# Kernel optimization log

Measured on AMD Instinct MI355X. Metric: run time of the kernel, lower is better.

The kernel has to match this reference:

```python
import jax, jax.numpy as jnp
import numpy as np

EPS = 1e-5
C = 64  # in_channels == feat_channels == out_channels


def _ln(x, g, b):
    m = jnp.mean(x, axis=-1, keepdims=True)
    v = jnp.mean(jnp.square(x - m), axis=-1, keepdims=True)
    return (x - m) * jax.lax.rsqrt(v + EPS) * g + b


def setup_inputs() -> dict:
    key = jax.random.key(0)
    ks = jax.random.split(key, 10)
    bs, nc, H, W = 8, 80, 256, 256
    d = {
        "feat": jax.random.normal(ks[0], (bs, C, H, W), jnp.float32),
        "head": jax.random.normal(ks[1], (bs, nc, C, 1), jnp.float32),
        "pred": jax.random.normal(ks[2], (bs, nc, H // 2, W // 2), jnp.float32),
        # linear transforms (stored [in, out], applied as x @ W + b)
        "W_pred_t": jax.random.normal(ks[3], (C, 2 * C), jnp.float32) * 0.05,
        "b_pred_t": jnp.zeros((2 * C,), jnp.float32),
        "W_head_t": jax.random.normal(ks[4], (C, 2 * C), jnp.float32) * 0.05,
        "b_head_t": jnp.zeros((2 * C,), jnp.float32),
        "W_pred_g": jax.random.normal(ks[5], (C, C), jnp.float32) * 0.05,
        "b_pred_g": jnp.zeros((C,), jnp.float32),
        "W_head_g": jax.random.normal(ks[6], (C, C), jnp.float32) * 0.05,
        "b_head_g": jnp.zeros((C,), jnp.float32),
        "W_fc": jax.random.normal(ks[7], (C, C), jnp.float32) * 0.05,
        "b_fc": jnp.zeros((C,), jnp.float32),
        # layernorm params
        "g_pin": jnp.ones((C,), jnp.float32), "be_pin": jnp.zeros((C,), jnp.float32),
        "g_hin": jnp.ones((C,), jnp.float32), "be_hin": jnp.zeros((C,), jnp.float32),
        "g_pout": jnp.ones((C,), jnp.float32), "be_pout": jnp.zeros((C,), jnp.float32),
        "g_hout": jnp.ones((C,), jnp.float32), "be_hout": jnp.zeros((C,), jnp.float32),
        "g_fc": jnp.ones((C,), jnp.float32), "be_fc": jnp.zeros((C,), jnp.float32),
    }
    return d


def reference(feat, head, pred,
              W_pred_t, b_pred_t, W_head_t, b_head_t,
              W_pred_g, b_pred_g, W_head_g, b_head_g,
              W_fc, b_fc,
              g_pin, be_pin, g_hin, be_hin,
              g_pout, be_pout, g_hout, be_hout,
              g_fc, be_fc):
    bs, nc = head.shape[:2]
    H, W = feat.shape[2], feat.shape[3]
    pred_up = jax.image.resize(pred, (bs, nc, H, W), method="bilinear")
    pred_up = jax.nn.sigmoid(pred_up)
    # head-aware feature assembly: [bs, nc, C]
    assemble = jnp.einsum("bnhw,bchw->bnc", pred_up, feat)
    a = assemble.reshape(-1, C)                      # [BN, C]
    BN = a.shape[0]
    # head: [bs, nc, C, kk] -> [BN, kk, C]
    hd = jnp.transpose(head.reshape(bs, nc, C, -1), (0, 1, 3, 2)).reshape(BN, -1, C)

    pf = a @ W_pred_t + b_pred_t                     # [BN, 2C]
    pf_in, pf_out = pf[:, :C], pf[:, C:]
    hf = hd @ W_head_t + b_head_t                    # [BN, kk, 2C]
    hf_in, hf_out = hf[..., :C], hf[..., C:]

    gate = hf_in * pf_in[:, None, :]                 # [BN, kk, C]
    head_gate = jax.nn.sigmoid(_ln(gate @ W_head_g + b_head_g, g_hin, be_hin))
    pred_gate = jax.nn.sigmoid(_ln(gate @ W_pred_g + b_pred_g, g_pin, be_pin))

    hf_out = _ln(hf_out, g_hout, be_hout)
    pf_out = _ln(pf_out, g_pout, be_pout)

    upd = pred_gate * pf_out[:, None, :] + head_gate * hf_out
    upd = jax.nn.relu(_ln(upd @ W_fc + b_fc, g_fc, be_fc))
    upd = upd.reshape(bs, nc, -1, C)
    upd = jnp.transpose(upd, (0, 1, 3, 2)).reshape(bs, nc, C, 1, 1)
    return upd
```

## Files before the change

### kernel.cpp

```cpp
#include <hip/hip_runtime.h>
#include <hip/hip_bf16.h>
#include <hip/hip_fp16.h>


using bf16x8 = __attribute__((ext_vector_type(8))) short;
using f32x4  = __attribute__((ext_vector_type(4))) float;

#define SCHED_FENCE() __builtin_amdgcn_sched_barrier(0)
#define LGKM_BARRIER() do { \
  asm volatile("s_waitcnt lgkmcnt(0)" ::: "memory"); \
  __builtin_amdgcn_s_barrier(); } while (0)

__device__ __forceinline__ unsigned pk2(float lo, float hi) {
  union { __hip_bfloat162 h2; unsigned u; } cv;
  cv.h2 = __float22bfloat162_rn(make_float2(lo, hi));
  return cv.u;
}
__device__ __forceinline__ float sigAB(float a, float b) {
  return __builtin_amdgcn_rcpf(1.0f + __builtin_amdgcn_exp2f(-0.36067376f * a - 1.08202128f * b));
}
__device__ __forceinline__ float sigBA(float a, float b) {
  return __builtin_amdgcn_rcpf(1.0f + __builtin_amdgcn_exp2f(-1.08202128f * a - 0.36067376f * b));
}

__global__ __launch_bounds__(256, 4) void k_assemble_half(
    const float* __restrict__ feat, const float* __restrict__ pred,
    __half* __restrict__ partial) {
  __shared__ __align__(16) unsigned short Pfrag[20 * 64 * 8];

  const int bid = blockIdx.x;
  const int wg  = (bid & 7) * 512 + (bid >> 3);
  const int half = wg & 1;
  const int h    = (wg >> 1) & 255;
  const int b    = wg >> 9;

  const int tid = threadIdx.x;
  const int gg = tid & 15, nbp = tid >> 4;
  const int wid = tid >> 6, l = tid & 63;
  const int ch16 = l & 15, kg = l >> 4, c0 = wid << 4;

  const int j = h >> 1;
  int r0, r1; float wy0, wy1;
  if ((h & 1) == 0) { r0 = (j > 0) ? j - 1 : 0; r1 = j; wy0 = 0.25f; wy1 = 0.75f; }
  else              { r0 = j; r1 = (j < 127) ? j + 1 : 127; wy0 = 0.75f; wy1 = 0.25f; }

  const int cbase = half << 6;
  const int csc   = 64 - half;
  const float* pbat = pred + (((size_t)(b * 80)) << 14);

  float4 p0[5], p1[5];
  #pragma unroll
  for (int i = 0; i < 5; ++i) {
    const float* pb = pbat + (((size_t)(nbp + 16 * i)) << 14);
    p0[i] = *(const float4*)(pb + (r0 << 7) + cbase + 4 * gg);
    p1[i] = *(const float4*)(pb + (r1 << 7) + cbase + 4 * gg);
  }

  #pragma unroll
  for (int i = 0; i < 5; ++i) {
    const int n = nbp + 16 * i;
    const float* pb = pbat + (((size_t)n) << 14);
    const float sc = wy0 * pb[(r0 << 7) + csc] + wy1 * pb[(r1 << 7) + csc];
    const float y0 = wy0 * p0[i].x + wy1 * p1[i].x;
    const float y1 = wy0 * p0[i].y + wy1 * p1[i].y;
    const float y2 = wy0 * p0[i].z + wy1 * p1[i].z;
    const float y3 = wy0 * p0[i].w + wy1 * p1[i].w;
    float yl = __shfl_up(y3, 1, 16);
    float yr = __shfl_down(y0, 1, 16);
    if (gg == 0)  yl = half ? sc : y0;
    if (gg == 15) yr = half ? y3 : sc;
    float P[8];
    P[0] = sigAB(yl, y0); P[1] = sigBA(y0, y1);
    P[2] = sigAB(y0, y1); P[3] = sigBA(y1, y2);
    P[4] = sigAB(y1, y2); P[5] = sigBA(y2, y3);
    P[6] = sigAB(y2, y3); P[7] = sigBA(y3, yr);
    uint4 s;
    s.x = pk2(P[0], P[1]); s.y = pk2(P[2], P[3]);
    s.z = pk2(P[4], P[5]); s.w = pk2(P[6], P[7]);
    const int ks = gg >> 2, kgw = gg & 3;
    const int slot = kgw * 16 + ((nbp ^ ks ^ (kgw << 1)) & 15);
    *(uint4*)&Pfrag[(((ks * 5 + i) * 64) + slot) * 8] = s;
  }
  __syncthreads();

  const float* fb = feat + (((size_t)(b * 64 + c0 + ch16)) << 16) + h * 256 + (half << 7);
  f32x4 acc[5] = {};
  #pragma unroll
  for (int ks = 0; ks < 4; ++ks) {
    const int pw = ks * 32 + kg * 8;
    const float4 f0 = *(const float4*)(fb + pw);
    const float4 f1 = *(const float4*)(fb + pw + 4);
    union { uint4 u; bf16x8 v; } bu;
    bu.u.x = pk2(f0.x, f0.y); bu.u.y = pk2(f0.z, f0.w);
    bu.u.z = pk2(f1.x, f1.y); bu.u.w = pk2(f1.z, f1.w);
    const int slot = kg * 16 + ((ch16 ^ ks ^ (kg << 1)) & 15);
    #pragma unroll
    for (int m = 0; m < 5; ++m) {
      const bf16x8 af = *(const bf16x8*)&Pfrag[(((ks * 5 + m) * 64) + slot) * 8];
      acc[m] = __builtin_amdgcn_mfma_f32_16x16x32_bf16(af, bu.v, acc[m], 0, 0, 0);
    }
  }

  __half* po = partial + ((size_t)(b * 512 + h * 2 + half)) * (80 * 64);
  #pragma unroll
  for (int m = 0; m < 5; ++m) {
    #pragma unroll
    for (int q = 0; q < 4; ++q) {
      const int n = m * 16 + kg * 4 + q;
      po[n * 64 + c0 + ch16] = __float2half(acc[m][q]);
    }
  }
}

__global__ __launch_bounds__(256) void k_assemble_full(
    const float* __restrict__ feat, const float* __restrict__ pred,
    __half* __restrict__ partial) {
  __shared__ __align__(16) unsigned short Pfrag[40 * 64 * 8];

  const int tid = threadIdx.x;
  const int b  = blockIdx.x >> 7;
  const int rb = blockIdx.x & 127;
  const int wid = tid >> 6, l = tid & 63;
  const int ch16 = l & 15, kg = l >> 4;
  const int c0 = wid << 4;
  const int h0 = rb * 2;
  const int gg = tid & 31, nb = tid >> 5;

  f32x4 acc[5] = {};
  const float* fwave = feat + (((size_t)(b * 64 + c0 + ch16)) << 16);
  const float* pbat  = pred + (((size_t)(b * 80)) << 14);

  #pragma unroll
  for (int r = 0; r < 2; ++r) {
    const int h = h0 + r;
    const int j = h >> 1;
    int r0, r1; float wy0, wy1;
    if ((h & 1) == 0) { r0 = (j > 0) ? j - 1 : 0; r1 = j; wy0 = 0.25f; wy1 = 0.75f; }
    else              { r0 = j; r1 = (j < 127) ? j + 1 : 127; wy0 = 0.75f; wy1 = 0.25f; }

    float4 p0[10], p1[10];
    #pragma unroll
    for (int i = 0; i < 10; ++i) {
      const float* pb = pbat + (((size_t)(nb + 8 * i)) << 14);
      p0[i] = *(const float4*)(pb + (r0 << 7) + gg * 4);
      p1[i] = *(const float4*)(pb + (r1 << 7) + gg * 4);
    }
    SCHED_FENCE();

    const float* fb = fwave + h * 256;
    float4 f[16];
    #pragma unroll
    for (int ks = 0; ks < 8; ++ks) {
      const int pw = ks * 32 + kg * 8;
      f[2 * ks]     = *(const float4*)(fb + pw);
      f[2 * ks + 1] = *(const float4*)(fb + pw + 4);
    }
    SCHED_FENCE();

    #pragma unroll
    for (int i = 0; i < 10; ++i) {
      const int n = nb + 8 * i;
      const float y0 = wy0 * p0[i].x + wy1 * p1[i].x;
      const float y1 = wy0 * p0[i].y + wy1 * p1[i].y;
      const float y2 = wy0 * p0[i].z + wy1 * p1[i].z;
      const float y3 = wy0 * p0[i].w + wy1 * p1[i].w;
      float yl = __shfl_up(y3, 1, 64);   if (gg == 0)  yl = y0;
      float yr = __shfl_down(y0, 1, 64); if (gg == 31) yr = y3;
      float P[8];
      P[0] = sigAB(yl, y0); P[1] = sigBA(y0, y1);
      P[2] = sigAB(y0, y1); P[3] = sigBA(y1, y2);
      P[4] = sigAB(y1, y2); P[5] = sigBA(y2, y3);
      P[6] = sigAB(y2, y3); P[7] = sigBA(y3, yr);
      uint4 s;
      s.x = pk2(P[0], P[1]); s.y = pk2(P[2], P[3]);
      s.z = pk2(P[4], P[5]); s.w = pk2(P[6], P[7]);
      const int ks = gg >> 2, kgw = gg & 3;
      const int slot = kgw * 16 + (((n & 15) ^ ks ^ (kgw << 1)) & 15);
      *(uint4*)&Pfrag[(((ks * 5 + (n >> 4)) * 64) + slot) * 8] = s;
    }
    LGKM_BARRIER();

    #pragma unroll
    for (int ks = 0; ks < 8; ++ks) {
      const float4 f0 = f[2 * ks], f1 = f[2 * ks + 1];
      union { uint4 u; bf16x8 v; } bu;
      bu.u.x = pk2(f0.x, f0.y); bu.u.y = pk2(f0.z, f0.w);
      bu.u.z = pk2(f1.x, f1.y); bu.u.w = pk2(f1.z, f1.w);
      const int slot = kg * 16 + ((ch16 ^ ks ^ (kg << 1)) & 15);
      #pragma unroll
      for (int m = 0; m < 5; ++m) {
        const bf16x8 af = *(const bf16x8*)&Pfrag[(((ks * 5 + m) * 64) + slot) * 8];
        acc[m] = __builtin_amdgcn_mfma_f32_16x16x32_bf16(af, bu.v, acc[m], 0, 0, 0);
      }
    }
    LGKM_BARRIER();
  }

  __half* po = partial + ((size_t)(b * 128 + rb)) * (80 * 64);
  #pragma unroll
  for (int m = 0; m < 5; ++m) {
    #pragma unroll
    for (int q = 0; q < 4; ++q) {
      const int n = m * 16 + kg * 4 + q;
      po[n * 64 + c0 + ch16] = __float2half(acc[m][q]);
    }
  }
}

__device__ __forceinline__ float wred64(float v) {
  #pragma unroll
  for (int off = 32; off > 0; off >>= 1) v += __shfl_xor(v, off, 64);
  return v;
}
__device__ __forceinline__ float lnorm(float x, const float* __restrict__ g,
                                       const float* __restrict__ be, int l) {
  const float m = wred64(x) * 0.015625f;
  const float d = x - m;
  const float var = wred64(d * d) * 0.015625f;
  return d * rsqrtf(var + 1e-5f) * g[l] + be[l];
}
__device__ __forceinline__ float sigmf(float x) {
  return __builtin_amdgcn_rcpf(1.0f + __builtin_amdgcn_exp2f(-1.44269504f * x));
}

__global__ __launch_bounds__(256) void k_head(
    const __half* __restrict__ partial, const float* __restrict__ head,
    const float* __restrict__ Wpt, const float* __restrict__ bpt,
    const float* __restrict__ Wht, const float* __restrict__ bht,
    const float* __restrict__ Wpg, const float* __restrict__ bpg,
    const float* __restrict__ Whg, const float* __restrict__ bhg,
    const float* __restrict__ Wfc, const float* __restrict__ bfc,
    const float* __restrict__ g_pin, const float* __restrict__ be_pin,
    const float* __restrict__ g_hin, const float* __restrict__ be_hin,
    const float* __restrict__ g_pout, const float* __restrict__ be_pout,
    const float* __restrict__ g_hout, const float* __restrict__ be_hout,
    const float* __restrict__ g_fc, const float* __restrict__ be_fc,
    float* __restrict__ out, int npart) {
  __shared__ float red[4][64];
  __shared__ float buf[4][64];
  const int tid = threadIdx.x, c = tid & 63, q = tid >> 6;
  const int r = blockIdx.x;
  const int b = r / 80, n = r % 80;
  const int npq = npart >> 2;

  const __half* pp = partial + ((size_t)b * npart + (size_t)q * npq) * 5120 + n * 64 + c;
  float s = 0.f;
  #pragma unroll 8
  for (int jj = 0; jj < npq; ++jj) s += __half2float(pp[(size_t)jj * 5120]);
  red[q][c] = s;
  __syncthreads();

  if (q == 0) {
    const float a_c = red[0][c] + red[1][c] + red[2][c] + red[3][c];
    buf[0][c] = a_c;
    buf[1][c] = head[(size_t)r * 64 + c];

    float pf_in = bpt[c], pf_out = bpt[64 + c];
    float hf_in = bht[c], hf_out = bht[64 + c];
    #pragma unroll 8
    for (int k = 0; k < 64; ++k) {
      const float av = buf[0][k];
      const float hv = buf[1][k];
      pf_in  += av * Wpt[k * 128 + c];
      pf_out += av * Wpt[k * 128 + 64 + c];
      hf_in  += hv * Wht[k * 128 + c];
      hf_out += hv * Wht[k * 128 + 64 + c];
    }
    buf[2][c] = hf_in * pf_in;

    float hg = bhg[c], pg = bpg[c];
    #pragma unroll 8
    for (int k = 0; k < 64; ++k) {
      const float gv = buf[2][k];
      hg += gv * Whg[k * 64 + c];
      pg += gv * Wpg[k * 64 + c];
    }
    const float head_gate = sigmf(lnorm(hg, g_hin, be_hin, c));
    const float pred_gate = sigmf(lnorm(pg, g_pin, be_pin, c));
    const float hfo = lnorm(hf_out, g_hout, be_hout, c);
    const float pfo = lnorm(pf_out, g_pout, be_pout, c);
    buf[3][c] = pred_gate * pfo + head_gate * hfo;

    float fc = bfc[c];
    #pragma unroll 8
    for (int k = 0; k < 64; ++k)
      fc += buf[3][k] * Wfc[k * 64 + c];
    float o = lnorm(fc, g_fc, be_fc, c);
    out[(size_t)r * 64 + c] = fmaxf(o, 0.f);
  }
}

extern "C" void kernel_launch(void* const* d_in, const int* in_sizes, int n_in,
                              void* d_out, int out_size, void* d_ws, size_t ws_size,
                              hipStream_t stream) {
  const float* feat   = (const float*)d_in[0];
  const float* head   = (const float*)d_in[1];
  const float* pred   = (const float*)d_in[2];
  const float* Wpt    = (const float*)d_in[3];
  const float* bpt    = (const float*)d_in[4];
  const float* Wht    = (const float*)d_in[5];
  const float* bht    = (const float*)d_in[6];
  const float* Wpg    = (const float*)d_in[7];
  const float* bpg    = (const float*)d_in[8];
  const float* Whg    = (const float*)d_in[9];
  const float* bhg    = (const float*)d_in[10];
  const float* Wfc    = (const float*)d_in[11];
  const float* bfc    = (const float*)d_in[12];
  const float* g_pin  = (const float*)d_in[13];
  const float* be_pin = (const float*)d_in[14];
  const float* g_hin  = (const float*)d_in[15];
  const float* be_hin = (const float*)d_in[16];
  const float* g_pout = (const float*)d_in[17];
  const float* be_pout= (const float*)d_in[18];
  const float* g_hout = (const float*)d_in[19];
  const float* be_hout= (const float*)d_in[20];
  const float* g_fc   = (const float*)d_in[21];
  const float* be_fc  = (const float*)d_in[22];
  float* out = (float*)d_out;
  __half* partial = (__half*)d_ws;

  const bool big = ws_size >= (size_t)8 * 512 * 5120 * 2;
  const int npart = big ? 512 : 128;

  if (big)
    hipLaunchKernelGGL(k_assemble_half, dim3(4096), dim3(256), 0, stream,
                       feat, pred, partial);
  else
    hipLaunchKernelGGL(k_assemble_full, dim3(1024), dim3(256), 0, stream,
                       feat, pred, partial);

  hipLaunchKernelGGL(k_head, dim3(640), dim3(256), 0, stream,
                     partial, head, Wpt, bpt, Wht, bht, Wpg, bpg, Whg, bhg,
                     Wfc, bfc, g_pin, be_pin, g_hin, be_hin, g_pout, be_pout,
                     g_hout, be_hout, g_fc, be_fc, out, npart);
}
```

Before: 60.70 us.

## Process output row pairs per block sharing pred rows and accumulators

Each assemble block now handles two adjacent upsampled rows (2j, 2j+1) instead of one. It reuses the shared middle pred row, prefetches the third row while the first MFMA pass runs, and accumulates both rows into one accumulator. This halves the grid and the partial-sum buffer, so the head kernel reduces over 256 partials instead of 512. The cost is an extra barrier and more registers per block, and there is half as much parallelism across blocks.

```diff
diff --git a/kernel.cpp b/kernel.cpp
--- a/kernel.cpp
+++ b/kernel.cpp
@@ -23,48 +23,50 @@
   return __builtin_amdgcn_rcpf(1.0f + __builtin_amdgcn_exp2f(-1.08202128f * a - 0.36067376f * b));
 }
 
-__global__ __launch_bounds__(256, 4) void k_assemble_half(
+__global__ __launch_bounds__(256, 4) void k_assemble_pair(
     const float* __restrict__ feat, const float* __restrict__ pred,
     __half* __restrict__ partial) {
   __shared__ __align__(16) unsigned short Pfrag[20 * 64 * 8];
 
   const int bid = blockIdx.x;
-  const int wg  = (bid & 7) * 512 + (bid >> 3);
+  const int wg  = (bid & 7) * 256 + (bid >> 3);
   const int half = wg & 1;
-  const int h    = (wg >> 1) & 255;
-  const int b    = wg >> 9;
+  const int jp   = (wg >> 1) & 127;
+  const int b    = wg >> 8;
 
   const int tid = threadIdx.x;
   const int gg = tid & 15, nbp = tid >> 4;
   const int wid = tid >> 6, l = tid & 63;
   const int ch16 = l & 15, kg = l >> 4, c0 = wid << 4;
 
-  const int j = h >> 1;
-  int r0, r1; float wy0, wy1;
-  if ((h & 1) == 0) { r0 = (j > 0) ? j - 1 : 0; r1 = j; wy0 = 0.25f; wy1 = 0.75f; }
-  else              { r0 = j; r1 = (j < 127) ? j + 1 : 127; wy0 = 0.75f; wy1 = 0.25f; }
+  const int rA = (jp > 0) ? jp - 1 : 0;
+  const int rB = jp;
+  const int rC = (jp < 127) ? jp + 1 : 127;
 
   const int cbase = half << 6;
   const int csc   = 64 - half;
   const float* pbat = pred + (((size_t)(b * 80)) << 14);
-
+  const float* fbase = feat + (((size_t)(b * 64 + c0 + ch16)) << 16) + (half << 7);
+
+  f32x4 acc[5] = {};
   float4 p0[5], p1[5];
+  float s0[5], s1[5];
+
   #pragma unroll
   for (int i = 0; i < 5; ++i) {
     const float* pb = pbat + (((size_t)(nbp + 16 * i)) << 14);
-    p0[i] = *(const float4*)(pb + (r0 << 7) + cbase + 4 * gg);
-    p1[i] = *(const float4*)(pb + (r1 << 7) + cbase + 4 * gg);
-  }
-
+    p0[i] = *(const float4*)(pb + (rA << 7) + cbase + 4 * gg);
+    p1[i] = *(const float4*)(pb + (rB << 7) + cbase + 4 * gg);
+    s0[i] = pb[(rA << 7) + csc];
+    s1[i] = pb[(rB << 7) + csc];
+  }
   #pragma unroll
   for (int i = 0; i < 5; ++i) {
-    const int n = nbp + 16 * i;
-    const float* pb = pbat + (((size_t)n) << 14);
-    const float sc = wy0 * pb[(r0 << 7) + csc] + wy1 * pb[(r1 << 7) + csc];
-    const float y0 = wy0 * p0[i].x + wy1 * p1[i].x;
-    const float y1 = wy0 * p0[i].y + wy1 * p1[i].y;
-    const float y2 = wy0 * p0[i].z + wy1 * p1[i].z;
-    const float y3 = wy0 * p0[i].w + wy1 * p1[i].w;
+    const float sc = 0.25f * s0[i] + 0.75f * s1[i];
+    const float y0 = 0.25f * p0[i].x + 0.75f * p1[i].x;
+    const float y1 = 0.25f * p0[i].y + 0.75f * p1[i].y;
+    const float y2 = 0.25f * p0[i].z + 0.75f * p1[i].z;
+    const float y3 = 0.25f * p0[i].w + 0.75f * p1[i].w;
     float yl = __shfl_up(y3, 1, 16);
     float yr = __shfl_down(y0, 1, 16);
     if (gg == 0)  yl = half ? sc : y0;
@@ -83,25 +85,78 @@
   }
   __syncthreads();
 
-  const float* fb = feat + (((size_t)(b * 64 + c0 + ch16)) << 16) + h * 256 + (half << 7);
-  f32x4 acc[5] = {};
-  #pragma unroll
-  for (int ks = 0; ks < 4; ++ks) {
-    const int pw = ks * 32 + kg * 8;
-    const float4 f0 = *(const float4*)(fb + pw);
-    const float4 f1 = *(const float4*)(fb + pw + 4);
-    union { uint4 u; bf16x8 v; } bu;
-    bu.u.x = pk2(f0.x, f0.y); bu.u.y = pk2(f0.z, f0.w);
-    bu.u.z = pk2(f1.x, f1.y); bu.u.w = pk2(f1.z, f1.w);
-    const int slot = kg * 16 + ((ch16 ^ ks ^ (kg << 1)) & 15);
-    #pragma unroll
-    for (int m = 0; m < 5; ++m) {
-      const bf16x8 af = *(const bf16x8*)&Pfrag[(((ks * 5 + m) * 64) + slot) * 8];
-      acc[m] = __builtin_amdgcn_mfma_f32_16x16x32_bf16(af, bu.v, acc[m], 0, 0, 0);
-    }
-  }
-
-  __half* po = partial + ((size_t)(b * 512 + h * 2 + half)) * (80 * 64);
+  #pragma unroll
+  for (int i = 0; i < 5; ++i) {
+    const float* pb = pbat + (((size_t)(nbp + 16 * i)) << 14);
+    p0[i] = *(const float4*)(pb + (rC << 7) + cbase + 4 * gg);
+    s0[i] = pb[(rC << 7) + csc];
+  }
+
+  {
+    const float* fb = fbase + (2 * jp) * 256;
+    #pragma unroll
+    for (int ks = 0; ks < 4; ++ks) {
+      const int pw = ks * 32 + kg * 8;
+      const float4 f0 = *(const float4*)(fb + pw);
+      const float4 f1 = *(const float4*)(fb + pw + 4);
+      union { uint4 u; bf16x8 v; } bu;
+      bu.u.x = pk2(f0.x, f0.y); bu.u.y = pk2(f0.z, f0.w);
+      bu.u.z = pk2(f1.x, f1.y); bu.u.w = pk2(f1.z, f1.w);
+      const int slot = kg * 16 + ((ch16 ^ ks ^ (kg << 1)) & 15);
+      #pragma unroll
+      for (int m = 0; m < 5; ++m) {
+        const bf16x8 af = *(const bf16x8*)&Pfrag[(((ks * 5 + m) * 64) + slot) * 8];
+        acc[m] = __builtin_amdgcn_mfma_f32_16x16x32_bf16(af, bu.v, acc[m], 0, 0, 0);
+      }
+    }
+  }
+  __syncthreads();
+
+  #pragma unroll
+  for (int i = 0; i < 5; ++i) {
+    const float sc = 0.25f * s0[i] + 0.75f * s1[i];
+    const float y0 = 0.25f * p0[i].x + 0.75f * p1[i].x;
+    const float y1 = 0.25f * p0[i].y + 0.75f * p1[i].y;
+    const float y2 = 0.25f * p0[i].z + 0.75f * p1[i].z;
+    const float y3 = 0.25f * p0[i].w + 0.75f * p1[i].w;
+    float yl = __shfl_up(y3, 1, 16);
+    float yr = __shfl_down(y0, 1, 16);
+    if (gg == 0)  yl = half ? sc : y0;
+    if (gg == 15) yr = half ? y3 : sc;
+    float P[8];
+    P[0] = sigAB(yl, y0); P[1] = sigBA(y0, y1);
+    P[2] = sigAB(y0, y1); P[3] = sigBA(y1, y2);
+    P[4] = sigAB(y1, y2); P[5] = sigBA(y2, y3);
+    P[6] = sigAB(y2, y3); P[7] = sigBA(y3, yr);
+    uint4 s;
+    s.x = pk2(P[0], P[1]); s.y = pk2(P[2], P[3]);
+    s.z = pk2(P[4], P[5]); s.w = pk2(P[6], P[7]);
+    const int ks = gg >> 2, kgw = gg & 3;
+    const int slot = kgw * 16 + ((nbp ^ ks ^ (kgw << 1)) & 15);
+    *(uint4*)&Pfrag[(((ks * 5 + i) * 64) + slot) * 8] = s;
+  }
+  __syncthreads();
+
+  {
+    const float* fb = fbase + (2 * jp + 1) * 256;
+    #pragma unroll
+    for (int ks = 0; ks < 4; ++ks) {
+      const int pw = ks * 32 + kg * 8;
+      const float4 f0 = *(const float4*)(fb + pw);
+      const float4 f1 = *(const float4*)(fb + pw + 4);
+      union { uint4 u; bf16x8 v; } bu;
+      bu.u.x = pk2(f0.x, f0.y); bu.u.y = pk2(f0.z, f0.w);
+      bu.u.z = pk2(f1.x, f1.y); bu.u.w = pk2(f1.z, f1.w);
+      const int slot = kg * 16 + ((ch16 ^ ks ^ (kg << 1)) & 15);
+      #pragma unroll
+      for (int m = 0; m < 5; ++m) {
+        const bf16x8 af = *(const bf16x8*)&Pfrag[(((ks * 5 + m) * 64) + slot) * 8];
+        acc[m] = __builtin_amdgcn_mfma_f32_16x16x32_bf16(af, bu.v, acc[m], 0, 0, 0);
+      }
+    }
+  }
+
+  __half* po = partial + ((size_t)(b * 256 + jp * 2 + half)) * (80 * 64);
   #pragma unroll
   for (int m = 0; m < 5; ++m) {
     #pragma unroll
@@ -189,7 +244,7 @@
       const int slot = kg * 16 + ((ch16 ^ ks ^ (kg << 1)) & 15);
       #pragma unroll
       for (int m = 0; m < 5; ++m) {
-        const bf16x8 af = *(const bf16x8*)&Pfrag[(((ks * 5 + m) * 64) + slot) * 8];
+        const bf16x8 af = *(const bf16x8*)&Pfrag[(((ks * 5 + (m)) * 64) + slot) * 8];
         acc[m] = __builtin_amdgcn_mfma_f32_16x16x32_bf16(af, bu.v, acc[m], 0, 0, 0);
       }
     }
@@ -319,11 +374,11 @@
   float* out = (float*)d_out;
   __half* partial = (__half*)d_ws;
 
-  const bool big = ws_size >= (size_t)8 * 512 * 5120 * 2;
-  const int npart = big ? 512 : 128;
+  const bool big = ws_size >= (size_t)8 * 256 * 5120 * 2;
+  const int npart = big ? 256 : 128;
 
   if (big)
-    hipLaunchKernelGGL(k_assemble_half, dim3(4096), dim3(256), 0, stream,
+    hipLaunchKernelGGL(k_assemble_pair, dim3(2048), dim3(256), 0, stream,
                        feat, pred, partial);
   else
     hipLaunchKernelGGL(k_assemble_full, dim3(1024), dim3(256), 0, stream,
```

Result: faster. 55.13 us (-9.2%).
